# Kernel tuning notes

Measured on AMD Instinct MI355X. Metric: run time of the kernel, lower is better.

Reference implementation:

```python
import jax, jax.numpy as jnp
import numpy as np

B, D, N_CAT, S = 8192, 128, 8192, 4
EPS = 1e-12  # F.normalize eps


def setup_inputs() -> dict:
    key = jax.random.key(0)
    k1, k2, k3, k4 = jax.random.split(key, 4)
    return {
        "batch_x": jax.random.normal(k1, (B, D), dtype=jnp.float32),
        "cat": jax.random.normal(k2, (N_CAT, D), dtype=jnp.float32),
        "y": jax.random.uniform(k3, (N_CAT,), dtype=jnp.float32),
        "phi": jax.random.normal(k4, (S, D), dtype=jnp.float32) * (6.0 / (D + 1)) ** 0.5,  # xavier-ish scale
        "bias": jnp.zeros((1,), dtype=jnp.float32),
    }


def reference(batch_x, cat, y, phi, bias):
    # con[n, b] = cat[n] . batch_x[b]   -> [N_cat, B]
    con = cat @ batch_x.T
    # F.normalize(con, p=4, dim=0): divide each column by its 4-norm (clamped)
    norm4 = jnp.sum(jnp.abs(con) ** 4, axis=0, keepdims=True) ** 0.25
    con = con / jnp.maximum(norm4, EPS)
    con = jax.nn.softmax(con, axis=0)
    s = phi.shape[0]
    c = con.shape[0] // s
    psi = con.reshape(s, c, con.shape[1])      # source_size chunks of [C, B]
    y_r = y.reshape(s, c)                      # source_size chunks of labels
    theta = jnp.exp(batch_x @ phi.T).T         # [S, B], raw exp (theta/sum_src unused in original)
    # sum over sources and chunk rows of y[s,c] * psi[s,c,b] * theta[s,b]
    y_hat = jnp.einsum('sc,scb,sb->b', y_r, psi, theta) + bias
    return y_hat
```

## Files before the change

### kernel.cpp

```cpp
#include <hip/hip_runtime.h>
#include <hip/hip_bf16.h>
#include <math.h>

typedef __bf16 bf16x8 __attribute__((ext_vector_type(8)));
typedef float f32x4 __attribute__((ext_vector_type(4)));

namespace {
constexpr int BN   = 8192;
constexpr int DK   = 128;
constexpr int NCAT = 8192;
constexpr int SRC  = 4;
constexpr int RG   = 16;
constexpr int TROWS = 64;
constexpr int NT   = 8;
constexpr float LOG2E = 1.4426950408889634f;
}

__device__ __forceinline__ float4 ld4(const float* p) {
    return *reinterpret_cast<const float4*>(p);
}

__device__ __forceinline__ void load_lds16(const unsigned short* g, unsigned short* l) {
    __builtin_amdgcn_global_load_lds(
        (const __attribute__((address_space(1))) void*)g,
        (__attribute__((address_space(3))) void*)l, 16, 0, 0);
}

__global__ __launch_bounds__(256) void k_convert2(const float* __restrict__ x,
                                                  const float* __restrict__ cat,
                                                  unsigned short* __restrict__ xb,
                                                  unsigned short* __restrict__ catb) {
    const int i = blockIdx.x * 256 + threadIdx.x;
    const int nx = BN * DK / 8;
    const float* src;
    unsigned short* dst;
    int j;
    size_t dchunk;
    if (i < nx) {
        src = x; dst = xb; j = i; dchunk = (size_t)j;
    } else {
        src = cat; dst = catb; j = i - nx;
        const int r = j >> 4, c = j & 15;
        const int rt = r >> 6, r6 = r & 63;
        dchunk = (size_t)rt * 1024 + r6 * 16 + (c ^ (r6 & 7));
    }
    const float4 a = ld4(src + (size_t)j * 8);
    const float4 b = ld4(src + (size_t)j * 8 + 4);
    float vals[8] = {a.x, a.y, a.z, a.w, b.x, b.y, b.z, b.w};
    union { unsigned short u[8]; uint4 v; } o;
#pragma unroll
    for (int q = 0; q < 8; ++q) {
        __hip_bfloat16 h = __float2bfloat16(vals[q]);
        o.u[q] = *reinterpret_cast<unsigned short*>(&h);
    }
    *reinterpret_cast<uint4*>(&dst[dchunk * 8]) = o.v;
}

template <int PASS>
__global__ __launch_bounds__(256, 3) void k_pass(
    const unsigned short* __restrict__ xb,
    const unsigned short* __restrict__ catb,
    const float* __restrict__ y,
    const float* __restrict__ pp4in,
    float* __restrict__ outA,
    float* __restrict__ outB) {
    __shared__ __align__(16) unsigned short As[2][TROWS * DK];
    __shared__ float nsh[128];
    __shared__ float redA[2][128];
    __shared__ float redB[2][128];

    const int t = threadIdx.x;
    const int colbase = blockIdx.x * 128;
    const int rowgrp = blockIdx.y;
    const int rowbase = rowgrp * 512;
    const int tile0 = rowgrp * NT;

    const int wid = t >> 6;
    const int rh = wid >> 1;
    const int ch = wid & 1;
    const int lane = t & 63;
    const int lr = lane & 15;
    const int kb = lane >> 4;

#pragma unroll
    for (int q = 0; q < 4; ++q)
        load_lds16(catb + ((size_t)tile0 * 1024 + (wid * 4 + q) * 64 + lane) * 8,
                   &As[0][(wid * 4 + q) * 64 * 8]);

    bf16x8 Bf[4][4];
#pragma unroll
    for (int j = 0; j < 4; ++j)
#pragma unroll
        for (int kk = 0; kk < 4; ++kk)
            Bf[j][kk] = *reinterpret_cast<const bf16x8*>(
                &xb[(size_t)(colbase + ch * 64 + j * 16 + lr) * DK + kk * 32 + kb * 8]);
#pragma unroll
    for (int j = 0; j < 4; ++j)
#pragma unroll
        for (int kk = 0; kk < 4; ++kk)
            asm volatile("" : "+v"(Bf[j][kk]));

    if (PASS == 2 && t < 128) {
        float sp = 0.f;
#pragma unroll
        for (int r = 0; r < RG; ++r) sp += pp4in[r * BN + colbase + t];
        nsh[t] = LOG2E / fmaxf(sqrtf(sqrtf(sp)), 1e-12f);
    }
    __syncthreads();

    float inm[4];
    if (PASS == 2) {
#pragma unroll
        for (int j = 0; j < 4; ++j) inm[j] = nsh[ch * 64 + j * 16 + lr];
    }

    float accA[4] = {0.f, 0.f, 0.f, 0.f};
    float accB[4] = {0.f, 0.f, 0.f, 0.f};

    for (int tl = 0; tl < NT; ++tl) {
        const int cur = tl & 1, nxt = cur ^ 1;
        if (tl < NT - 1) {
#pragma unroll
            for (int q = 0; q < 4; ++q)
                load_lds16(catb + ((size_t)(tile0 + tl + 1) * 1024 +
                                   (wid * 4 + q) * 64 + lane) * 8,
                           &As[nxt][(wid * 4 + q) * 64 * 8]);
        }
        float4 yv0, yv1;
        if (PASS == 2) {
            yv0 = ld4(&y[rowbase + tl * 64 + rh * 32 + kb * 4]);
            yv1 = ld4(&y[rowbase + tl * 64 + rh * 32 + 16 + kb * 4]);
        }

        bf16x8 a[2][4];
#pragma unroll
        for (int i = 0; i < 2; ++i) {
            const int row = rh * 32 + i * 16 + lr;
#pragma unroll
            for (int kk = 0; kk < 4; ++kk)
                a[i][kk] = *reinterpret_cast<const bf16x8*>(
                    &As[cur][row * 128 + (((kk * 4 + kb) ^ (lr & 7)) * 8)]);
        }

        f32x4 acc[2][4];
#pragma unroll
        for (int i = 0; i < 2; ++i)
#pragma unroll
            for (int j = 0; j < 4; ++j) acc[i][j] = (f32x4){0.f, 0.f, 0.f, 0.f};
#pragma unroll
        for (int kk = 0; kk < 4; ++kk)
#pragma unroll
            for (int i = 0; i < 2; ++i)
#pragma unroll
                for (int j = 0; j < 4; ++j)
                    acc[i][j] = __builtin_amdgcn_mfma_f32_16x16x32_bf16(
                        a[i][kk], Bf[j][kk], acc[i][j], 0, 0, 0);

        if (PASS == 1) {
#pragma unroll
            for (int i = 0; i < 2; ++i)
#pragma unroll
                for (int j = 0; j < 4; ++j)
#pragma unroll
                    for (int r = 0; r < 4; ++r) {
                        const float v = acc[i][j][r];
                        const float v2 = v * v;
                        accA[j] = fmaf(v2, v2, accA[j]);
                    }
        } else {
#pragma unroll
            for (int i = 0; i < 2; ++i) {
                const float4 yv = (i == 0) ? yv0 : yv1;
                const float yr4[4] = {yv.x, yv.y, yv.z, yv.w};
#pragma unroll
                for (int r = 0; r < 4; ++r) {
                    const float yr = yr4[r];
#pragma unroll
                    for (int j = 0; j < 4; ++j) {
                        const float e = exp2f(acc[i][j][r] * inm[j]);
                        accA[j] += e;
                        accB[j] = fmaf(yr, e, accB[j]);
                    }
                }
            }
        }
        __syncthreads();
    }

#pragma unroll
    for (int j = 0; j < 4; ++j) {
        accA[j] += __shfl_xor(accA[j], 16, 64);
        accA[j] += __shfl_xor(accA[j], 32, 64);
        if (PASS == 2) {
            accB[j] += __shfl_xor(accB[j], 16, 64);
            accB[j] += __shfl_xor(accB[j], 32, 64);
        }
    }
    if (lane < 16) {
#pragma unroll
        for (int j = 0; j < 4; ++j) {
            redA[rh][ch * 64 + j * 16 + lane] = accA[j];
            if (PASS == 2) redB[rh][ch * 64 + j * 16 + lane] = accB[j];
        }
    }
    __syncthreads();
    if (t < 128) {
        outA[(size_t)rowgrp * BN + colbase + t] = redA[0][t] + redA[1][t];
        if (PASS == 2)
            outB[(size_t)rowgrp * BN + colbase + t] = redB[0][t] + redB[1][t];
    }
}

__global__ __launch_bounds__(256) void k_final(const float* __restrict__ x,
                                               const float* __restrict__ phi,
                                               const float* __restrict__ pZ,
                                               const float* __restrict__ pW,
                                               const float* __restrict__ bias,
                                               float* __restrict__ out) {
    const int g = blockIdx.x * 256 + threadIdx.x;
    const int b = g >> 2, s = g & 3;
    float dot = 0.f;
#pragma unroll
    for (int k = 0; k < DK; k += 4) {
        const float4 xv = ld4(&x[(size_t)b * DK + k]);
        const float4 pv = ld4(&phi[s * DK + k]);
        dot += xv.x * pv.x + xv.y * pv.y + xv.z * pv.z + xv.w * pv.w;
    }
    float W = 0.f, Z = 0.f;
#pragma unroll
    for (int r = 0; r < 4; ++r) {
        W += pW[(size_t)(4 * s + r) * BN + b];
        Z += pZ[(size_t)(4 * s + r) * BN + b];
    }
    float v = __expf(dot) * W;
    v += __shfl_xor(v, 1, 64);
    v += __shfl_xor(v, 2, 64);
    Z += __shfl_xor(Z, 1, 64);
    Z += __shfl_xor(Z, 2, 64);
    if (s == 0) out[b] = v / Z + bias[0];
}

extern "C" void kernel_launch(void* const* d_in, const int* in_sizes, int n_in,
                              void* d_out, int out_size, void* d_ws, size_t ws_size,
                              hipStream_t stream) {
    const float* x    = (const float*)d_in[0];
    const float* cat  = (const float*)d_in[1];
    const float* y    = (const float*)d_in[2];
    const float* phi  = (const float*)d_in[3];
    const float* bias = (const float*)d_in[4];
    float* out = (float*)d_out;

    char* ws = (char*)d_ws;
    unsigned short* xb   = (unsigned short*)ws;
    unsigned short* catb = xb + (size_t)BN * DK;
    float* pp4 = (float*)(catb + (size_t)NCAT * DK);
    float* pZ  = pp4 + (size_t)RG * BN;
    float* pW  = pZ + (size_t)RG * BN;

    k_convert2<<<(BN * DK + NCAT * DK) / 8 / 256, 256, 0, stream>>>(x, cat, xb, catb);
    k_pass<1><<<dim3(BN / 128, RG), 256, 0, stream>>>(xb, catb, y, nullptr, pp4, nullptr);
    k_pass<2><<<dim3(BN / 128, RG), 256, 0, stream>>>(xb, catb, y, pp4, pZ, pW);
    k_final<<<BN * SRC / 256, 256, 0, stream>>>(x, phi, pZ, pW, bias, out);
}
```

Before: 73.21 us.

## Triple-buffer LDS tile staging with explicit vmcnt waits and preloaded y

Switches the cat-tile LDS staging from double to triple buffering, prefetching two tiles ahead. The per-iteration __syncthreads is replaced with a manual s_waitcnt vmcnt plus s_barrier. The y labels for the row group are preloaded into shared memory instead of being read from global memory every iteration, and MFMA issue priority is raised around the matrix loop. The aim is to hide global-to-LDS latency and cut barrier stalls, at the cost of more LDS per block, which may reduce occupancy. The hand-written vmcnt count also depends on the exact number of outstanding loads, so it is fragile.

```diff
diff --git a/kernel.cpp b/kernel.cpp
--- a/kernel.cpp
+++ b/kernel.cpp
@@ -24,6 +24,14 @@
     __builtin_amdgcn_global_load_lds(
         (const __attribute__((address_space(1))) void*)g,
         (__attribute__((address_space(3))) void*)l, 16, 0, 0);
+}
+
+__device__ __forceinline__ void stage_tile(const unsigned short* __restrict__ src,
+                                           unsigned short* dst, int wid, int lane) {
+#pragma unroll
+    for (int q = 0; q < 4; ++q)
+        load_lds16(src + ((size_t)((wid * 4 + q) * 64 + lane)) * 8,
+                   dst + (size_t)(wid * 4 + q) * 512);
 }
 
 __global__ __launch_bounds__(256) void k_convert2(const float* __restrict__ x,
@@ -64,7 +72,8 @@
     const float* __restrict__ pp4in,
     float* __restrict__ outA,
     float* __restrict__ outB) {
-    __shared__ __align__(16) unsigned short As[2][TROWS * DK];
+    __shared__ __align__(16) unsigned short As[3][TROWS * DK];
+    __shared__ float ysh[512];
     __shared__ float nsh[128];
     __shared__ float redA[2][128];
     __shared__ float redB[2][128];
@@ -72,7 +81,6 @@
     const int t = threadIdx.x;
     const int colbase = blockIdx.x * 128;
     const int rowgrp = blockIdx.y;
-    const int rowbase = rowgrp * 512;
     const int tile0 = rowgrp * NT;
 
     const int wid = t >> 6;
@@ -82,11 +90,6 @@
     const int lr = lane & 15;
     const int kb = lane >> 4;
 
-#pragma unroll
-    for (int q = 0; q < 4; ++q)
-        load_lds16(catb + ((size_t)tile0 * 1024 + (wid * 4 + q) * 64 + lane) * 8,
-                   &As[0][(wid * 4 + q) * 64 * 8]);
-
     bf16x8 Bf[4][4];
 #pragma unroll
     for (int j = 0; j < 4; ++j)
@@ -100,13 +103,22 @@
         for (int kk = 0; kk < 4; ++kk)
             asm volatile("" : "+v"(Bf[j][kk]));
 
-    if (PASS == 2 && t < 128) {
-        float sp = 0.f;
-#pragma unroll
-        for (int r = 0; r < RG; ++r) sp += pp4in[r * BN + colbase + t];
-        nsh[t] = LOG2E / fmaxf(sqrtf(sqrtf(sp)), 1e-12f);
-    }
-    __syncthreads();
+    if (PASS == 2) {
+        if (t < 128) {
+            float sp = 0.f;
+#pragma unroll
+            for (int r = 0; r < RG; ++r) sp += pp4in[r * BN + colbase + t];
+            nsh[t] = LOG2E / fmaxf(sqrtf(sqrtf(sp)), 1e-12f);
+        }
+#pragma unroll
+        for (int q = t; q < 512; q += 256) ysh[q] = y[rowgrp * 512 + q];
+    }
+
+    stage_tile(catb + (size_t)tile0 * 8192, &As[0][0], wid, lane);
+    stage_tile(catb + (size_t)(tile0 + 1) * 8192, &As[1][0], wid, lane);
+
+    asm volatile("s_waitcnt lgkmcnt(0)" ::: "memory");
+    __builtin_amdgcn_s_barrier();
 
     float inm[4];
     if (PASS == 2) {
@@ -117,20 +129,16 @@
     float accA[4] = {0.f, 0.f, 0.f, 0.f};
     float accB[4] = {0.f, 0.f, 0.f, 0.f};
 
+#pragma unroll
     for (int tl = 0; tl < NT; ++tl) {
-        const int cur = tl & 1, nxt = cur ^ 1;
-        if (tl < NT - 1) {
-#pragma unroll
-            for (int q = 0; q < 4; ++q)
-                load_lds16(catb + ((size_t)(tile0 + tl + 1) * 1024 +
-                                   (wid * 4 + q) * 64 + lane) * 8,
-                           &As[nxt][(wid * 4 + q) * 64 * 8]);
-        }
-        float4 yv0, yv1;
-        if (PASS == 2) {
-            yv0 = ld4(&y[rowbase + tl * 64 + rh * 32 + kb * 4]);
-            yv1 = ld4(&y[rowbase + tl * 64 + rh * 32 + 16 + kb * 4]);
-        }
+        if (tl < NT - 1)
+            asm volatile("s_waitcnt vmcnt(4)" ::: "memory");
+        else
+            asm volatile("s_waitcnt vmcnt(0)" ::: "memory");
+        __builtin_amdgcn_s_barrier();
+        if (tl < NT - 2)
+            stage_tile(catb + (size_t)(tile0 + tl + 2) * 8192,
+                       &As[(tl + 2) % 3][0], wid, lane);
 
         bf16x8 a[2][4];
 #pragma unroll
@@ -139,7 +147,7 @@
 #pragma unroll
             for (int kk = 0; kk < 4; ++kk)
                 a[i][kk] = *reinterpret_cast<const bf16x8*>(
-                    &As[cur][row * 128 + (((kk * 4 + kb) ^ (lr & 7)) * 8)]);
+                    &As[tl % 3][row * 128 + (((kk * 4 + kb) ^ (lr & 7)) * 8)]);
         }
 
         f32x4 acc[2][4];
@@ -147,6 +155,8 @@
         for (int i = 0; i < 2; ++i)
 #pragma unroll
             for (int j = 0; j < 4; ++j) acc[i][j] = (f32x4){0.f, 0.f, 0.f, 0.f};
+
+        __builtin_amdgcn_s_setprio(1);
 #pragma unroll
         for (int kk = 0; kk < 4; ++kk)
 #pragma unroll
@@ -155,6 +165,7 @@
                 for (int j = 0; j < 4; ++j)
                     acc[i][j] = __builtin_amdgcn_mfma_f32_16x16x32_bf16(
                         a[i][kk], Bf[j][kk], acc[i][j], 0, 0, 0);
+        __builtin_amdgcn_s_setprio(0);
 
         if (PASS == 1) {
 #pragma unroll
@@ -170,7 +181,8 @@
         } else {
 #pragma unroll
             for (int i = 0; i < 2; ++i) {
-                const float4 yv = (i == 0) ? yv0 : yv1;
+                const float4 yv = *reinterpret_cast<const float4*>(
+                    &ysh[tl * 64 + rh * 32 + i * 16 + kb * 4]);
                 const float yr4[4] = {yv.x, yv.y, yv.z, yv.w};
 #pragma unroll
                 for (int r = 0; r < 4; ++r) {
@@ -184,7 +196,6 @@
                 }
             }
         }
-        __syncthreads();
     }
 
 #pragma unroll
```

New measurement: 68.95 us. 1.06x faster.
